# Optimization experiments

Measured on AMD Instinct MI355X. Metric: run time of the kernel, lower is better.

## Reference

```python
import jax, jax.numpy as jnp
from jax import lax
import numpy as np

N, C, H, W = 8, 32, 64, 64
KS, NB = 7, 6            # kernel_size, num_bases
TB = (KS // 2) * NB      # total_bases = 18
BC = TB * NB             # bc_dim = 108
INTER = max(64, BC // 2) # 64
OUT = 64
PAD = KS // 2
EPS = 1e-5


def conv3x3(x, w, b):
    # x: (N,Cin,H,W), w: (Cout,Cin,3,3)
    y = lax.conv_general_dilated(x, w, (1, 1), [(1, 1), (1, 1)],
                                 dimension_numbers=('NCHW', 'OIHW', 'NCHW'))
    return y + b[None, :, None, None]


def batchnorm(x, g, b):
    # training-mode BN: batch stats over (N,H,W)
    mu = jnp.mean(x, axis=(0, 2, 3), keepdims=True)
    var = jnp.var(x, axis=(0, 2, 3), keepdims=True)
    return (x - mu) * lax.rsqrt(var + EPS) * g[None, :, None, None] + b[None, :, None, None]


def setup_inputs() -> dict:
    key = jax.random.key(0)
    ks = jax.random.split(key, 12)
    s = 0.05
    # random bases as in get_random_bases: (TB, KS*KS), zero-mean-ish rows
    f = jax.random.normal(ks[0], (TB, KS * KS), dtype=jnp.float32)
    bases = f - jnp.mean(f, axis=1, keepdims=True) / jnp.std(f, axis=1, keepdims=True)
    return {
        'x': jax.random.normal(ks[1], (N, C, H, W), dtype=jnp.float32),
        'conv1_w': jax.random.normal(ks[2], (INTER, C, 3, 3), dtype=jnp.float32) * s,
        'conv1_b': jax.random.normal(ks[3], (INTER,), dtype=jnp.float32) * s,
        'bn1_g': jnp.ones((INTER,), jnp.float32),
        'bn1_b': jnp.zeros((INTER,), jnp.float32),
        'conv2_w': jax.random.normal(ks[4], (BC, INTER, 3, 3), dtype=jnp.float32) * s,
        'conv2_b': jax.random.normal(ks[5], (BC,), dtype=jnp.float32) * s,
        'bn2_g': jnp.ones((BC,), jnp.float32),
        'bn2_b': jnp.zeros((BC,), jnp.float32),
        'bases': bases,
        'out_w': jax.random.normal(ks[6], (OUT, C * NB), dtype=jnp.float32) * s,
        'out_b': jax.random.normal(ks[7], (OUT,), dtype=jnp.float32) * s,
    }


def reference(x, conv1_w, conv1_b, bn1_g, bn1_b, conv2_w, conv2_b,
              bn2_g, bn2_b, bases, out_w, out_b):
    # bases_net: conv3x3 -> BN -> tanh -> conv3x3 -> BN -> tanh
    h = jnp.tanh(batchnorm(conv3x3(x, conv1_w, conv1_b), bn1_g, bn1_b))
    coef = jnp.tanh(batchnorm(conv3x3(h, conv2_w, conv2_b), bn2_g, bn2_b))
    # (N, BC, H, W) -> (N, NB, TB, H, W) -> (N, H, W, NB, TB)
    coef = coef.reshape(N, NB, TB, H, W).transpose(0, 3, 4, 1, 2)
    # atoms: (coef[...,None] * bases).sum(-2).transpose(-1,-2) => (N,H,W,KS^2,NB)
    atoms = jnp.einsum('nhwmt,tk->nhwkm', coef, bases)
    # unfold: channel-major (C, ks, ks) flattened, matching F.unfold
    patches = lax.conv_general_dilated_patches(
        x, (KS, KS), (1, 1), [(PAD, PAD), (PAD, PAD)],
        dimension_numbers=('NCHW', 'OIHW', 'NCHW'))  # (N, C*KS*KS, H, W)
    patches = patches.reshape(N, C, KS * KS, H, W)
    # per-pixel contraction over ks^2: (N,H,W,C,NB)
    bases_out = jnp.einsum('nckhw,nhwkm->nhwcm', patches, atoms)
    bases_out = bases_out.reshape(N, H, W, C * NB)
    out = jnp.einsum('nhwd,od->nohw', bases_out, out_w) + out_b[None, :, None, None]
    return out
```

## Files before the change

### kernel.cpp

```cpp
#include <hip/hip_runtime.h>
#include <hip/hip_bf16.h>

#define N_ 8
#define C_ 32
#define H_ 64
#define W_ 64
#define HW_ (H_*W_)
#define NHW_ (N_*HW_)
#define INTER_ 64
#define BC_ 108
#define KS_ 7
#define K2_ (KS_*KS_)
#define NB_ 6
#define TB_ 18
#define OUT_ 64
#define DDIM_ (C_*NB_)
#define P2CH_ 288

typedef __attribute__((ext_vector_type(8))) short short8;
typedef __attribute__((ext_vector_type(4))) float f32x4;
typedef __attribute__((ext_vector_type(2))) float f32x2;

__device__ __forceinline__ unsigned short f2bf(float f) {
    union { float f; unsigned u; } v; v.f = f;
    unsigned r = v.u + 0x7fffu + ((v.u >> 16) & 1u);
    return (unsigned short)(r >> 16);
}
__device__ __forceinline__ float bf2f(unsigned short h) {
    return __uint_as_float((unsigned int)h << 16);
}

__device__ __forceinline__ short8 frag4(const unsigned int* p) {
    union { unsigned int u[4]; short8 s; } v;
    v.u[0] = p[0]; v.u[1] = p[1]; v.u[2] = p[2]; v.u[3] = p[3];
    return v.s;
}

template<int TP0, int NTP>
__device__ __forceinline__ void pconv_pass(const float (*sx)[44],
                                           const float* __restrict__ bases,
                                           unsigned int* __restrict__ P2,
                                           int n, int c, int r0, int rb, int lane) {
    f32x2 av[NTP][4];
    #pragma unroll
    for (int tp = 0; tp < NTP; tp++)
        #pragma unroll
        for (int rr = 0; rr < 4; rr++) av[tp][rr] = (f32x2){0.f, 0.f};

    #pragma unroll 1
    for (int kx = 0; kx < 7; kx++) {
        float rw[12];
        const float* sp = &sx[lane + kx][rb];
        #pragma unroll
        for (int qq = 0; qq < 3; qq++) {
            float4 r4 = *(const float4*)(sp + qq * 4);
            rw[qq * 4 + 0] = r4.x; rw[qq * 4 + 1] = r4.y;
            rw[qq * 4 + 2] = r4.z; rw[qq * 4 + 3] = r4.w;
        }
        #pragma unroll
        for (int tp = 0; tp < NTP; tp++) {
            #pragma unroll
            for (int ky = 0; ky < 7; ky++) {
                f32x2 w2;
                w2.x = bases[(2 * (TP0 + tp)) * K2_ + ky * 7 + kx];
                w2.y = bases[(2 * (TP0 + tp) + 1) * K2_ + ky * 7 + kx];
                #pragma unroll
                for (int rr = 0; rr < 4; rr++) {
                    float xv = rw[rr + ky];
                    f32x2 xv2 = (f32x2){xv, xv};
                    av[tp][rr] += xv2 * w2;
                }
            }
        }
    }

    #pragma unroll
    for (int tp = 0; tp < NTP; tp++)
        #pragma unroll
        for (int rr = 0; rr < 4; rr++) {
            int gr = r0 + rb + rr;
            unsigned int pk = (unsigned int)f2bf(av[tp][rr].x) |
                              ((unsigned int)f2bf(av[tp][rr].y) << 16);
            P2[(((size_t)n * P2CH_ + (TP0 + tp) * 32 + c) << 12) + (gr << 6) + lane] = pk;
        }
}

__global__ __launch_bounds__(256) void k_front(const float* __restrict__ x,
                                               const float* __restrict__ bases,
                                               const float* __restrict__ w1,
                                               const float* __restrict__ w2,
                                               const float* __restrict__ ow,
                                               const float* __restrict__ b1,
                                               unsigned short* __restrict__ wb2,
                                               unsigned short* __restrict__ wbp,
                                               unsigned int* __restrict__ P2,
                                               float* __restrict__ y1,
                                               float2* __restrict__ part1) {
    __shared__ __align__(16) char smem[39936];
    int bid = blockIdx.x, t = threadIdx.x;

    if (bid < 1024) {
        float (*sx)[44] = (float(*)[44])smem;
        int rq = bid & 3;
        int c  = (bid >> 2) & 31;
        int n  = bid >> 7;
        int lane = t & 63, wv = t >> 6;
        int r0 = rq << 4;

        const float* xc = x + (((size_t)n * C_ + c) << 12);
        #pragma unroll
        for (int j = 0; j < 6; j++) {
            int p = wv + 4 * j;
            if (p < 22) {
                int grow = r0 - 3 + p;
                bool rowok = (grow >= 0 && grow < H_);
                int wx = lane - 3;
                float v = 0.f;
                if (rowok && wx >= 0) v = xc[(grow << 6) + wx];
                sx[lane][p] = v;
                if (lane < 6) {
                    int wx2 = 61 + lane;
                    float v2 = 0.f;
                    if (rowok && wx2 < W_) v2 = xc[(grow << 6) + wx2];
                    sx[64 + lane][p] = v2;
                }
            }
        }
        __syncthreads();

        int rb = wv * 4;
        pconv_pass<0, 5>(sx, bases, P2, n, c, r0, rb, lane);
        pconv_pass<5, 4>(sx, bases, P2, n, c, r0, rb, lane);
    } else if (bid < 2048) {
        unsigned short* sx1 = (unsigned short*)smem;
        unsigned short* sw1 = sx1 + 198 * 40;
        float* sbp = (float*)(sw1 + 9 * 32 * 40);

        int cid = bid - 1024;
        int n = cid >> 7;
        int rem = cid & 127;
        int co0 = (rem & 1) << 5;
        int h0 = rem >> 1;
        int lane = t & 63, wv = t >> 6;
        int q = lane >> 4, n15 = lane & 15;

        if (t < 96) {
            int c = t & 31, r = t >> 5;
            int hh = h0 - 1 + r;
            bool rok = (hh >= 0 && hh < H_);
            const float* xr = x + (((size_t)n * C_ + c) << 12) + (hh << 6);
            sx1[(r * 66 + 0) * 40 + c] = 0;
            sx1[(r * 66 + 65) * 40 + c] = 0;
            #pragma unroll 4
            for (int col = 1; col <= 64; col++) {
                float v = rok ? xr[col - 1] : 0.f;
                sx1[(r * 66 + col) * 40 + c] = f2bf(v);
            }
        }
        for (int e = t; e < 9 * 32 * 32; e += 256) {
            int ci = e & 31, co = (e >> 5) & 31, s = e >> 10;
            sw1[(s * 32 + co) * 40 + ci] = f2bf(w1[(((co0 + co) << 5) + ci) * 9 + s]);
        }
        __syncthreads();

        f32x4 acc[2];
        acc[0] = (f32x4){0.f, 0.f, 0.f, 0.f};
        acc[1] = (f32x4){0.f, 0.f, 0.f, 0.f};
        #pragma unroll
        for (int s = 0; s < 9; s++) {
            int dy = s / 3, dx = s % 3;
            short8 bfr = *(const short8*)(sx1 + (dy * 66 + wv * 16 + n15 + dx) * 40 + q * 8);
            #pragma unroll
            for (int mt = 0; mt < 2; mt++) {
                short8 afr = *(const short8*)(sw1 + (s * 32 + mt * 16 + n15) * 40 + q * 8);
                acc[mt] = __builtin_amdgcn_mfma_f32_16x16x32_bf16(afr, bfr, acc[mt], 0, 0, 0);
            }
        }

        int wcol = wv * 16 + n15;
        float sa[2][4], sa2[2][4];
        #pragma unroll
        for (int mt = 0; mt < 2; mt++)
            #pragma unroll
            for (int reg = 0; reg < 4; reg++) {
                int co = co0 + mt * 16 + q * 4 + reg;
                float v = acc[mt][reg] + b1[co];
                y1[(((size_t)n * INTER_ + co) << 12) + (h0 << 6) + wcol] = v;
                sa[mt][reg] = v; sa2[mt][reg] = v * v;
            }
        #pragma unroll
        for (int mt = 0; mt < 2; mt++)
            #pragma unroll
            for (int reg = 0; reg < 4; reg++) {
                float s = sa[mt][reg], s2 = sa2[mt][reg];
                #pragma unroll
                for (int off = 1; off < 16; off <<= 1) {
                    s += __shfl_xor(s, off);
                    s2 += __shfl_xor(s2, off);
                }
                if (n15 == 0) {
                    int cl = mt * 16 + q * 4 + reg;
                    sbp[wv * 64 + cl * 2] = s;
                    sbp[wv * 64 + cl * 2 + 1] = s2;
                }
            }
        __syncthreads();
        if (t < 32) {
            float s = 0.f, s2 = 0.f;
            #pragma unroll
            for (int w = 0; w < 4; w++) { s += sbp[w * 64 + t * 2]; s2 += sbp[w * 64 + t * 2 + 1]; }
            atomicAdd(&part1[((co0 + t) << 3) + n].x, s);
            atomicAdd(&part1[((co0 + t) << 3) + n].y, s2);
        }
    } else {
        int pbid = bid - 2048;
        if (pbid < 288) {
            int i = pbid * 256 + t;
            int ci = i & 63, co = (i >> 6) & 127, s = i >> 13;
            unsigned short v = 0;
            if (co < BC_) v = f2bf(w2[((co << 6) + ci) * 9 + s]);
            wb2[i] = v;
        } else {
            int i = (pbid - 288) * 256 + t;
            if (i < OUT_ * DDIM_) {
                float v = ow[i];
                unsigned short hi = f2bf(v);
                wbp[i] = hi;
                wbp[OUT_ * DDIM_ + i] = f2bf(v - bf2f(hi));
            }
        }
    }
}

template<int CIN, int COG, int ROWS, int WPAD, int NCOQ>
__global__ __launch_bounds__(256) void k_conv3(const unsigned short* __restrict__ xb,
                                               const unsigned short* __restrict__ wb,
                                               const float* __restrict__ bias,
                                               float* __restrict__ y,
                                               float2* __restrict__ part,
                                               int COUT_real) {
    constexpr int CPAD = CIN + 8;
    constexpr int NSLC = (ROWS + 2) * 66;
    constexpr int MT = COG / 16;
    constexpr int NTW = ROWS;
    constexpr int KSTEPS = CIN / 32;
    __shared__ unsigned short sx[NSLC * CPAD];
    __shared__ unsigned short sw[9 * COG * CPAD];
    __shared__ float sbp[4][COG * 2];

    int bid = blockIdx.x;
    int coq = bid % NCOQ;
    int rp = (bid / NCOQ) % (H_ / ROWS);
    int n = bid / (NCOQ * (H_ / ROWS));
    int h0 = rp * ROWS;
    int co0 = coq * COG;
    int t = threadIdx.x;
    int lane = t & 63, wv = t >> 6;
    int q = lane >> 4, n15 = lane & 15;

    {
        const unsigned int* xg = (const unsigned int*)xb + (size_t)n * HW_ * (CIN / 2);
        unsigned int* sxd = (unsigned int*)sx;
        constexpr int DW = CIN / 2;
        constexpr int DWPT = DW / 8;
        int part_ = t & 7;
        for (int sl = (t >> 3); sl < NSLC; sl += 32) {
            int r = sl / 66, col = sl % 66;
            int hh = h0 - 1 + r, ww = col - 1;
            unsigned int v[DWPT];
            #pragma unroll
            for (int i = 0; i < DWPT; i++) v[i] = 0;
            if (hh >= 0 && hh < H_ && ww >= 0 && ww < W_) {
                const unsigned int* gp = xg + (size_t)(hh * W_ + ww) * DW + part_ * DWPT;
                #pragma unroll
                for (int i = 0; i < DWPT; i++) v[i] = gp[i];
            }
            unsigned int* d = sxd + sl * (CPAD / 2) + part_ * DWPT;
            #pragma unroll
            for (int i = 0; i < DWPT; i++) d[i] = v[i];
        }
    }
    {
        const unsigned int* wg = (const unsigned int*)wb;
        unsigned int* swd = (unsigned int*)sw;
        constexpr int TOT = 9 * COG * (CIN / 2);
        for (int e = t; e < TOT; e += 256) {
            int s_co = e / (CIN / 2), cw = e % (CIN / 2);
            int s = s_co / COG, co = s_co % COG;
            swd[s_co * (CPAD / 2) + cw] = wg[((size_t)s * WPAD + co0 + co) * (CIN / 2) + cw];
        }
    }
    __syncthreads();

    f32x4 acc[NTW][MT];
    #pragma unroll
    for (int a = 0; a < NTW; a++)
        #pragma unroll
        for (int m = 0; m < MT; m++) acc[a][m] = (f32x4){0.f, 0.f, 0.f, 0.f};

    #pragma unroll
    for (int s = 0; s < 9; s++) {
        int dy = s / 3, dx = s % 3;
        #pragma unroll
        for (int kc = 0; kc < KSTEPS; kc++) {
            int ci0 = kc * 32;
            short8 bfr[NTW];
            #pragma unroll
            for (int ntl = 0; ntl < NTW; ntl++) {
                int nt = wv * NTW + ntl;
                int r_out = nt >> 2, col0 = (nt & 3) * 16;
                bfr[ntl] = *(const short8*)(sx + ((r_out + dy) * 66 + col0 + n15 + dx) * CPAD + ci0 + q * 8);
            }
            #pragma unroll
            for (int mt = 0; mt < MT; mt++) {
                short8 afr = *(const short8*)(sw + ((s * COG) + mt * 16 + n15) * CPAD + ci0 + q * 8);
                #pragma unroll
                for (int ntl = 0; ntl < NTW; ntl++)
                    acc[ntl][mt] = __builtin_amdgcn_mfma_f32_16x16x32_bf16(afr, bfr[ntl], acc[ntl][mt], 0, 0, 0);
            }
        }
    }

    float sacc[MT][4], sacc2[MT][4];
    #pragma unroll
    for (int mt = 0; mt < MT; mt++)
        #pragma unroll
        for (int reg = 0; reg < 4; reg++) { sacc[mt][reg] = 0.f; sacc2[mt][reg] = 0.f; }

    #pragma unroll
    for (int ntl = 0; ntl < NTW; ntl++) {
        int nt = wv * NTW + ntl;
        int h = h0 + (nt >> 2), wcol = (nt & 3) * 16 + n15;
        #pragma unroll
        for (int mt = 0; mt < MT; mt++) {
            #pragma unroll
            for (int reg = 0; reg < 4; reg++) {
                int co = co0 + mt * 16 + q * 4 + reg;
                if (co < COUT_real) {
                    float v = acc[ntl][mt][reg] + bias[co];
                    y[(((size_t)n * COUT_real + co) << 12) + h * W_ + wcol] = v;
                    sacc[mt][reg] += v;
                    sacc2[mt][reg] += v * v;
                }
            }
        }
    }

    #pragma unroll
    for (int mt = 0; mt < MT; mt++)
        #pragma unroll
        for (int reg = 0; reg < 4; reg++) {
            float s = sacc[mt][reg], s2 = sacc2[mt][reg];
            #pragma unroll
            for (int off = 1; off < 16; off <<= 1) {
                s += __shfl_xor(s, off);
                s2 += __shfl_xor(s2, off);
            }
            if (n15 == 0) {
                int cl = mt * 16 + q * 4 + reg;
                sbp[wv][cl * 2] = s;
                sbp[wv][cl * 2 + 1] = s2;
            }
        }
    __syncthreads();
    if (t < COG) {
        float s = 0.f, s2 = 0.f;
        #pragma unroll
        for (int w2 = 0; w2 < 4; w2++) { s += sbp[w2][t * 2]; s2 += sbp[w2][t * 2 + 1]; }
        int co = co0 + t;
        if (co < COUT_real) {
            atomicAdd(&part[(co << 3) + n].x, s);
            atomicAdd(&part[(co << 3) + n].y, s2);
        }
    }
}

__global__ __launch_bounds__(256) void k_bntr(const float* __restrict__ y1,
                                              const float2* __restrict__ part,
                                              const float* __restrict__ g,
                                              const float* __restrict__ bb,
                                              unsigned short* __restrict__ y1b) {
    __shared__ unsigned short sT[64 * 68];
    __shared__ float scs[INTER_], shs[INTER_];
    int bid = blockIdx.x, t = threadIdx.x;
    int n = bid >> 6, hw0 = (bid << 6) & 4095;
    if (t < INTER_) {
        float s = 0.f, s2 = 0.f;
        #pragma unroll
        for (int j = 0; j < 8; j++) { float2 p = part[t * 8 + j]; s += p.x; s2 += p.y; }
        float mu = s / (float)NHW_, var = s2 / (float)NHW_ - mu * mu;
        float sc = g[t] * rsqrtf(var + 1e-5f);
        scs[t] = sc; shs[t] = bb[t] - mu * sc;
    }
    __syncthreads();
    for (int i = t; i < 4096; i += 256) {
        int c = i >> 6, px = i & 63;
        float v = y1[(((size_t)n * INTER_ + c) << 12) + hw0 + px];
        sT[px * 68 + c] = f2bf(tanhf(v * scs[c] + shs[c]));
    }
    __syncthreads();
    unsigned int* yd = (unsigned int*)y1b;
    for (int i = t; i < 2048; i += 256) {
        int px = i >> 5, cw = i & 31;
        unsigned int lo = sT[px * 68 + cw * 2], hi = sT[px * 68 + cw * 2 + 1];
        yd[(((size_t)n << 12) + hw0 + px) * 32 + cw] = lo | (hi << 16);
    }
}

#define YPAD_ 97
__global__ __launch_bounds__(256) void k_ytail(const float* __restrict__ y2,
                                               const float2* __restrict__ part,
                                               const float* __restrict__ g,
                                               const float* __restrict__ bb,
                                               const unsigned int* __restrict__ P2,
                                               const unsigned short* __restrict__ wbp,
                                               const float* __restrict__ out_b,
                                               float* __restrict__ out) {
    __shared__ float scs[BC_], shs[BC_];
    __shared__ float cfs[BC_][32];
    __shared__ unsigned int sYh[32 * YPAD_];
    __shared__ unsigned int sYl[32 * YPAD_];

    int bid = blockIdx.x;
    int n = bid >> 7, px0 = (bid & 127) << 5;
    int t = threadIdx.x;

    int px = t & 31, cg = t >> 5;
    unsigned int u[4][9];
    {
        const unsigned int* Pb = P2 + (((size_t)n * P2CH_) << 12) + px0 + px;
        #pragma unroll
        for (int cc = 0; cc < 4; cc++) {
            int c = cg * 4 + cc;
            #pragma unroll
            for (int tp = 0; tp < 9; tp++)
                u[cc][tp] = Pb[(size_t)(tp * 32 + c) << 12];
        }
    }

    if (t < BC_) {
        float s = 0.f, s2 = 0.f;
        #pragma unroll
        for (int j = 0; j < 8; j++) { float2 p = part[t * 8 + j]; s += p.x; s2 += p.y; }
        float mu = s / (float)NHW_, var = s2 / (float)NHW_ - mu * mu;
        float sc = g[t] * rsqrtf(var + 1e-5f);
        scs[t] = sc; shs[t] = bb[t] - mu * sc;
    }
    __syncthreads();

    for (int i = t; i < BC_ * 32; i += 256) {
        int ch = i >> 5, pxx = i & 31;
        float v = y2[(((size_t)n * BC_ + ch) << 12) + px0 + pxx];
        cfs[ch][pxx] = tanhf(v * scs[ch] + shs[ch]);
    }
    __syncthreads();

    {
        f32x2 pv2[2][TB_];
        #pragma unroll
        for (int j = 0; j < 2; j++)
            #pragma unroll
            for (int tp = 0; tp < 9; tp++) {
                pv2[j][2 * tp].x     = __uint_as_float(u[2 * j][tp] << 16);
                pv2[j][2 * tp].y     = __uint_as_float(u[2 * j + 1][tp] << 16);
                pv2[j][2 * tp + 1].x = __uint_as_float(u[2 * j][tp] & 0xffff0000u);
                pv2[j][2 * tp + 1].y = __uint_as_float(u[2 * j + 1][tp] & 0xffff0000u);
            }
        f32x2 ym2[2][NB_];
        #pragma unroll
        for (int j = 0; j < 2; j++)
            #pragma unroll
            for (int m = 0; m < NB_; m++) ym2[j][m] = (f32x2){0.f, 0.f};
        #pragma unroll
        for (int m = 0; m < NB_; m++)
            #pragma unroll
            for (int tt = 0; tt < TB_; tt++) {
                float cfv = cfs[m * TB_ + tt][px];
                f32x2 c2 = (f32x2){cfv, cfv};
                ym2[0][m] += c2 * pv2[0][tt];
                ym2[1][m] += c2 * pv2[1][tt];
            }
        #pragma unroll
        for (int j = 0; j < 2; j++) {
            #pragma unroll
            for (int half = 0; half < 2; half++) {
                int c = cg * 4 + 2 * j + half;
                #pragma unroll
                for (int jj = 0; jj < 3; jj++) {
                    float y0 = half ? ym2[j][2 * jj].y     : ym2[j][2 * jj].x;
                    float y1v = half ? ym2[j][2 * jj + 1].y : ym2[j][2 * jj + 1].x;
                    unsigned short h0 = f2bf(y0);
                    unsigned short h1 = f2bf(y1v);
                    unsigned short l0 = f2bf(y0 - bf2f(h0));
                    unsigned short l1 = f2bf(y1v - bf2f(h1));
                    sYh[px * YPAD_ + c * 3 + jj] = (unsigned int)h0 | ((unsigned int)h1 << 16);
                    sYl[px * YPAD_ + c * 3 + jj] = (unsigned int)l0 | ((unsigned int)l1 << 16);
                }
            }
        }
    }
    __syncthreads();

    int lane = t & 63, wv = t >> 6;
    int q = lane >> 4, n15 = lane & 15;
    f32x4 acc[2];
    acc[0] = (f32x4){0.f, 0.f, 0.f, 0.f};
    acc[1] = (f32x4){0.f, 0.f, 0.f, 0.f};
    #pragma unroll
    for (int ks = 0; ks < 6; ks++) {
        short8 ah = *(const short8*)(wbp + (wv * 16 + n15) * DDIM_ + ks * 32 + q * 8);
        short8 al = *(const short8*)(wbp + OUT_ * DDIM_ + (wv * 16 + n15) * DDIM_ + ks * 32 + q * 8);
        #pragma unroll
        for (int nt = 0; nt < 2; nt++) {
            short8 bh = frag4(sYh + (nt * 16 + n15) * YPAD_ + ks * 16 + q * 4);
            short8 bl = frag4(sYl + (nt * 16 + n15) * YPAD_ + ks * 16 + q * 4);
            acc[nt] = __builtin_amdgcn_mfma_f32_16x16x32_bf16(ah, bh, acc[nt], 0, 0, 0);
            acc[nt] = __builtin_amdgcn_mfma_f32_16x16x32_bf16(ah, bl, acc[nt], 0, 0, 0);
            acc[nt] = __builtin_amdgcn_mfma_f32_16x16x32_bf16(al, bh, acc[nt], 0, 0, 0);
        }
    }
    #pragma unroll
    for (int nt = 0; nt < 2; nt++)
        #pragma unroll
        for (int reg = 0; reg < 4; reg++) {
            int o = wv * 16 + q * 4 + reg;
            out[(((size_t)n * OUT_ + o) << 12) + px0 + nt * 16 + n15] = acc[nt][reg] + out_b[o];
        }
}

extern "C" void kernel_launch(void* const* d_in, const int* in_sizes, int n_in,
                              void* d_out, int out_size, void* d_ws, size_t ws_size,
                              hipStream_t stream) {
    const float* x       = (const float*)d_in[0];
    const float* conv1_w = (const float*)d_in[1];
    const float* conv1_b = (const float*)d_in[2];
    const float* bn1_g   = (const float*)d_in[3];
    const float* bn1_b   = (const float*)d_in[4];
    const float* conv2_w = (const float*)d_in[5];
    const float* conv2_b = (const float*)d_in[6];
    const float* bn2_g   = (const float*)d_in[7];
    const float* bn2_b   = (const float*)d_in[8];
    const float* bases   = (const float*)d_in[9];
    const float* out_w   = (const float*)d_in[10];
    const float* out_b   = (const float*)d_in[11];
    float* out = (float*)d_out;

    float* y1  = (float*)d_ws;
    float* y2  = y1 + (size_t)N_ * INTER_ * HW_;
    unsigned int* P2 = (unsigned int*)(y2 + (size_t)N_ * BC_ * HW_);
    unsigned short* xb  = (unsigned short*)(P2 + (size_t)N_ * P2CH_ * HW_);
    unsigned short* y1b = xb + (size_t)NHW_ * C_;
    unsigned short* wb1 = y1b + (size_t)NHW_ * INTER_;
    unsigned short* wb2 = wb1 + 9 * 64 * 32;
    unsigned short* wbp = wb2 + 9 * 128 * 64;
    float2* part1 = (float2*)(wbp + 2 * OUT_ * DDIM_);
    float2* part2 = part1 + INTER_ * 8;

    hipMemsetAsync(part1, 0, (size_t)(INTER_ + BC_) * 8 * sizeof(float2), stream);

    k_front<<<2384, 256, 0, stream>>>(x, bases, conv1_w, conv2_w, out_w, conv1_b,
                                      wb2, wbp, P2, y1, part1);

    k_bntr<<<512, 256, 0, stream>>>(y1, part1, bn1_g, bn1_b, y1b);

    k_conv3<INTER_, 16, 2, 128, 7><<<N_ * 32 * 7, 256, 0, stream>>>(
        y1b, wb2, conv2_b, y2, part2, BC_);

    k_ytail<<<1024, 256, 0, stream>>>(y2, (const float2*)part2, bn2_g, bn2_b,
                                      P2, wbp, out_b, out);
}
```

Baseline: 216.6 us.

## Split weight prep into separate kernel and read conv1 weights from global bf16

Moves the bf16 conversion of conv1/conv2/output weights and the zeroing of the BN partial-sum buffer into a new small k_prep kernel, which replaces the memset. The conv1 blocks in k_front no longer convert and stage their 9x32x32 weight slice into shared memory. They read pre-converted bf16 weights straight from global memory for the MFMA A operand. Input staging now uses float4 loads spread across all threads. This shrinks shared memory per block, which should raise occupancy and remove redundant per-block weight conversion, at the cost of an extra launch and uncached global loads in the MFMA loop.

```diff
diff --git a/kernel.cpp b/kernel.cpp
--- a/kernel.cpp
+++ b/kernel.cpp
@@ -85,18 +85,45 @@
         }
 }
 
+__global__ __launch_bounds__(256) void k_prep(const float* __restrict__ w1,
+                                              const float* __restrict__ w2,
+                                              const float* __restrict__ ow,
+                                              unsigned short* __restrict__ wb1,
+                                              unsigned short* __restrict__ wb2,
+                                              unsigned short* __restrict__ wbp,
+                                              float* __restrict__ pz) {
+    int bid = blockIdx.x, t = threadIdx.x;
+    if (bid < 72) {
+        int i = bid * 256 + t;
+        int ci = i & 31, co = (i >> 5) & 63, s = i >> 11;
+        wb1[i] = f2bf(w1[((co << 5) + ci) * 9 + s]);
+    } else if (bid < 360) {
+        int i = (bid - 72) * 256 + t;
+        int ci = i & 63, co = (i >> 6) & 127, s = i >> 13;
+        unsigned short v = 0;
+        if (co < BC_) v = f2bf(w2[((co << 6) + ci) * 9 + s]);
+        wb2[i] = v;
+    } else if (bid < 408) {
+        int i = (bid - 360) * 256 + t;
+        if (i < OUT_ * DDIM_) {
+            float v = ow[i];
+            unsigned short hi = f2bf(v);
+            wbp[i] = hi;
+            wbp[OUT_ * DDIM_ + i] = f2bf(v - bf2f(hi));
+        }
+    } else {
+        for (int i = t; i < (INTER_ + BC_) * 8 * 2; i += 256) pz[i] = 0.f;
+    }
+}
+
 __global__ __launch_bounds__(256) void k_front(const float* __restrict__ x,
                                                const float* __restrict__ bases,
-                                               const float* __restrict__ w1,
-                                               const float* __restrict__ w2,
-                                               const float* __restrict__ ow,
+                                               const unsigned short* __restrict__ wb1,
                                                const float* __restrict__ b1,
-                                               unsigned short* __restrict__ wb2,
-                                               unsigned short* __restrict__ wbp,
                                                unsigned int* __restrict__ P2,
                                                float* __restrict__ y1,
                                                float2* __restrict__ part1) {
-    __shared__ __align__(16) char smem[39936];
+    __shared__ __align__(16) char smem[16896];
     int bid = blockIdx.x, t = threadIdx.x;
 
     if (bid < 1024) {
@@ -131,10 +158,9 @@
         int rb = wv * 4;
         pconv_pass<0, 5>(sx, bases, P2, n, c, r0, rb, lane);
         pconv_pass<5, 4>(sx, bases, P2, n, c, r0, rb, lane);
-    } else if (bid < 2048) {
+    } else {
         unsigned short* sx1 = (unsigned short*)smem;
-        unsigned short* sw1 = sx1 + 198 * 40;
-        float* sbp = (float*)(sw1 + 9 * 32 * 40);
+        float* sbp = (float*)(sx1 + 198 * 40);
 
         int cid = bid - 1024;
         int n = cid >> 7;
@@ -144,22 +170,23 @@
         int lane = t & 63, wv = t >> 6;
         int q = lane >> 4, n15 = lane & 15;
 
+        for (int e = t; e < 1536; e += 256) {
+            int c = e & 31, rc4 = e >> 5;
+            int r = rc4 >> 4, cq = rc4 & 15;
+            int hh = h0 - 1 + r;
+            bool rok = (hh >= 0 && hh < H_);
+            float4 v = {0.f, 0.f, 0.f, 0.f};
+            if (rok) v = *(const float4*)(x + (((size_t)n * C_ + c) << 12) + (hh << 6) + cq * 4);
+            unsigned short* d = sx1 + (r * 66 + 1 + cq * 4) * 40 + c;
+            d[0]   = f2bf(v.x);
+            d[40]  = f2bf(v.y);
+            d[80]  = f2bf(v.z);
+            d[120] = f2bf(v.w);
+        }
         if (t < 96) {
             int c = t & 31, r = t >> 5;
-            int hh = h0 - 1 + r;
-            bool rok = (hh >= 0 && hh < H_);
-            const float* xr = x + (((size_t)n * C_ + c) << 12) + (hh << 6);
             sx1[(r * 66 + 0) * 40 + c] = 0;
             sx1[(r * 66 + 65) * 40 + c] = 0;
-            #pragma unroll 4
-            for (int col = 1; col <= 64; col++) {
-                float v = rok ? xr[col - 1] : 0.f;
-                sx1[(r * 66 + col) * 40 + c] = f2bf(v);
-            }
-        }
-        for (int e = t; e < 9 * 32 * 32; e += 256) {
-            int ci = e & 31, co = (e >> 5) & 31, s = e >> 10;
-            sw1[(s * 32 + co) * 40 + ci] = f2bf(w1[(((co0 + co) << 5) + ci) * 9 + s]);
         }
         __syncthreads();
 
@@ -172,7 +199,7 @@
             short8 bfr = *(const short8*)(sx1 + (dy * 66 + wv * 16 + n15 + dx) * 40 + q * 8);
             #pragma unroll
             for (int mt = 0; mt < 2; mt++) {
-                short8 afr = *(const short8*)(sw1 + (s * 32 + mt * 16 + n15) * 40 + q * 8);
+                short8 afr = *(const short8*)(wb1 + s * 2048 + (co0 + mt * 16 + n15) * 32 + q * 8);
                 acc[mt] = __builtin_amdgcn_mfma_f32_16x16x32_bf16(afr, bfr, acc[mt], 0, 0, 0);
             }
         }
@@ -211,23 +238,6 @@
             for (int w = 0; w < 4; w++) { s += sbp[w * 64 + t * 2]; s2 += sbp[w * 64 + t * 2 + 1]; }
             atomicAdd(&part1[((co0 + t) << 3) + n].x, s);
             atomicAdd(&part1[((co0 + t) << 3) + n].y, s2);
-        }
-    } else {
-        int pbid = bid - 2048;
-        if (pbid < 288) {
-            int i = pbid * 256 + t;
-            int ci = i & 63, co = (i >> 6) & 127, s = i >> 13;
-            unsigned short v = 0;
-            if (co < BC_) v = f2bf(w2[((co << 6) + ci) * 9 + s]);
-            wb2[i] = v;
-        } else {
-            int i = (pbid - 288) * 256 + t;
-            if (i < OUT_ * DDIM_) {
-                float v = ow[i];
-                unsigned short hi = f2bf(v);
-                wbp[i] = hi;
-                wbp[OUT_ * DDIM_ + i] = f2bf(v - bf2f(hi));
-            }
         }
     }
 }
@@ -556,10 +566,10 @@
     float2* part1 = (float2*)(wbp + 2 * OUT_ * DDIM_);
     float2* part2 = part1 + INTER_ * 8;
 
-    hipMemsetAsync(part1, 0, (size_t)(INTER_ + BC_) * 8 * sizeof(float2), stream);
-
-    k_front<<<2384, 256, 0, stream>>>(x, bases, conv1_w, conv2_w, out_w, conv1_b,
-                                      wb2, wbp, P2, y1, part1);
+    k_prep<<<409, 256, 0, stream>>>(conv1_w, conv2_w, out_w, wb1, wb2, wbp,
+                                    (float*)part1);
+
+    k_front<<<2048, 256, 0, stream>>>(x, bases, wb1, conv1_b, P2, y1, part1);
 
     k_bntr<<<512, 256, 0, stream>>>(y1, part1, bn1_g, bn1_b, y1b);
 
```

After: 192.1 us. 1.13x faster.
